# Performance work log

Measured on AMD Instinct MI355X. Metric: run time of the kernel, lower is better.

Reference implementation:

```python
import jax, jax.numpy as jnp
import numpy as np

N, E, DIN, H, C = 100000, 1600000, 128, 4, 32
NEG_SLOPE = 0.2

def setup_inputs() -> dict:
    key = jax.random.key(0)
    ks = jax.random.split(key, 6)
    x = jax.random.normal(ks[0], (N, DIN), jnp.float32)
    edge_index = jax.random.randint(ks[1], (2, E), 0, N)
    # positive scalar edge weights (log2 is applied to them)
    edge_attr = jax.random.uniform(ks[2], (E,), jnp.float32, 0.05, 1.0)
    scale = 1.0 / np.sqrt(DIN).astype(np.float32)
    W = jax.random.normal(ks[3], (DIN, H * C), jnp.float32) * scale
    att_src = jax.random.normal(ks[4], (H, C), jnp.float32) * scale
    att_dst = jax.random.normal(ks[5], (H, C), jnp.float32) * scale
    bias = jnp.zeros((H * C,), jnp.float32)
    return {"x": x, "edge_index": edge_index, "edge_attr": edge_attr,
            "W": W, "att_src": att_src, "att_dst": att_dst, "bias": bias}

def _gat_forward(x, edge_attr, W, att_src, att_dst, bias, src, dst):
    n = x.shape[0]
    h = (x @ W).reshape(n, H, C)                      # [N,H,C]
    a_src = jnp.einsum('nhc,hc->nh', h, att_src)      # [N,H]
    a_dst = jnp.einsum('nhc,hc->nh', h, att_dst)      # [N,H]
    # add self loops (pyg GATConv default), edge weight fill_value='mean' over incoming edges
    deg = jax.ops.segment_sum(jnp.ones_like(edge_attr), dst, n)
    loop_w = jnp.where(deg > 0,
                       jax.ops.segment_sum(edge_attr, dst, n) / jnp.maximum(deg, 1.0),
                       1.0)
    loops = jnp.arange(n)
    src_full = jnp.concatenate([src, loops])
    dst_full = jnp.concatenate([dst, loops])
    w_full = jnp.concatenate([edge_attr, loop_w])
    # per-edge attention logits
    alpha = jax.nn.leaky_relu(a_src[src_full] + a_dst[dst_full], NEG_SLOPE)
    alpha = alpha + jnp.log2(w_full)[:, None]         # [E+N, H]
    # segment (per-target-node) softmax
    amax = jax.ops.segment_max(alpha, dst_full, n)    # [N,H]; every node has a self loop
    ex = jnp.exp(alpha - amax[dst_full])
    denom = jax.ops.segment_sum(ex, dst_full, n)
    alpha = ex / denom[dst_full]                      # dropout is identity in eval mode
    # scatter-aggregate messages
    out = jax.ops.segment_sum(h[src_full] * alpha[:, :, None], dst_full, n)  # [N,H,C]
    return out.reshape(n, H * C) + bias

def reference(x, edge_index, edge_attr, W, att_src, att_dst, bias):
    src, dst = edge_index[0], edge_index[1]
    return _gat_forward(x, edge_attr, W, att_src, att_dst, bias, src, dst)
```

## Files before the change

### kernel.cpp

```cpp
#include <hip/hip_runtime.h>
#include <math.h>

#define DIN 128
#define NH 4
#define HC 128
static constexpr float NEG_SLOPE = 0.2f;

typedef __attribute__((ext_vector_type(8))) short bf16x8;
typedef __attribute__((ext_vector_type(4))) float f32x4;

__device__ __forceinline__ float leaky(float x) { return x > 0.f ? x : NEG_SLOPE * x; }

__device__ __forceinline__ unsigned short f2bf(float f) {
  unsigned u = __float_as_uint(f);
  unsigned r = (u + 0x7fffu + ((u >> 16) & 1u)) >> 16;
  return (unsigned short)r;
}
__device__ __forceinline__ float bf_lo(unsigned u) { return __uint_as_float(u << 16); }
__device__ __forceinline__ float bf_hi(unsigned u) { return __uint_as_float(u & 0xffff0000u); }

__global__ void k_init(const float* __restrict__ W, short* __restrict__ bswz,
                       unsigned* __restrict__ cnt, int n) {
  int g = blockIdx.x * blockDim.x + threadIdx.x;
  if (g < n) cnt[g] = 0u;
  if (g < 2048) {
    int ntile = g >> 8;
    int ks = (g >> 6) & 3;
    int lane = g & 63;
    int col = (ntile << 4) + (lane & 15);
    int kb = ks * 32 + ((lane >> 4) << 3);
    bf16x8 v;
#pragma unroll
    for (int j = 0; j < 8; ++j) v[j] = (short)f2bf(W[(kb + j) * HC + col]);
    ((bf16x8*)bswz)[g] = v;
  }
}

__global__ __launch_bounds__(256) void k_fused(
    const float* __restrict__ x, const short* __restrict__ bswz,
    const float* __restrict__ att_s, const float* __restrict__ att_d,
    unsigned short* __restrict__ hbf,
    float* __restrict__ a_src, float* __restrict__ a_dst, int n,
    const int* __restrict__ dst,
    unsigned* __restrict__ cnt, unsigned short* __restrict__ rank,
    int E, int CB) {
  int grp = blockIdx.x / 5;
  int r = blockIdx.x % 5;
  if (r >= 3) {
    int cid = grp * 2 + (r - 3);
    int stride = CB * 256;
    for (int e = cid * 256 + (int)threadIdx.x; e < E; e += stride) {
      unsigned old = atomicAdd(&cnt[dst[e]], 1u);
      rank[e] = (unsigned short)old;
    }
    return;
  }
  int pid = grp * 3 + r;
  int wtile = pid * 4 + (threadIdx.x >> 6);
  int ntiles = n >> 4;
  if (wtile >= ntiles) return;
  int lane = threadIdx.x & 63;
  int row0 = wtile << 4;

  int arow = row0 + (lane & 15);
  int kbase = (lane >> 4) << 3;
  const float* xr = x + (size_t)arow * DIN;
  bf16x8 a[4];
#pragma unroll
  for (int ks = 0; ks < 4; ++ks) {
    float4 lo = *(const float4*)(xr + ks * 32 + kbase);
    float4 hi = *(const float4*)(xr + ks * 32 + kbase + 4);
    bf16x8 v;
    v[0] = (short)f2bf(lo.x); v[1] = (short)f2bf(lo.y);
    v[2] = (short)f2bf(lo.z); v[3] = (short)f2bf(lo.w);
    v[4] = (short)f2bf(hi.x); v[5] = (short)f2bf(hi.y);
    v[6] = (short)f2bf(hi.z); v[7] = (short)f2bf(hi.w);
    a[ks] = v;
  }

  const bf16x8* B = (const bf16x8*)bswz;
  int crow_base = row0 + ((lane >> 4) << 2);
  int ccol_off = lane & 15;

  float ra[4] = {0.f, 0.f, 0.f, 0.f};
  float rd[4] = {0.f, 0.f, 0.f, 0.f};

#pragma unroll
  for (int ntile = 0; ntile < 8; ++ntile) {
    f32x4 acc = {0.f, 0.f, 0.f, 0.f};
#pragma unroll
    for (int ks = 0; ks < 4; ++ks)
      acc = __builtin_amdgcn_mfma_f32_16x16x32_bf16(a[ks], B[(ntile * 4 + ks) * 64 + lane], acc, 0, 0, 0);
    int col = (ntile << 4) + ccol_off;
    float as = att_s[col], ad = att_d[col];
#pragma unroll
    for (int i = 0; i < 4; ++i) {
      hbf[(size_t)(crow_base + i) * HC + col] = f2bf(acc[i]);
      ra[i] = fmaf(acc[i], as, ra[i]);
      rd[i] = fmaf(acc[i], ad, rd[i]);
    }
    if (ntile & 1) {
      int hh = ntile >> 1;
#pragma unroll
      for (int i = 0; i < 4; ++i) {
#pragma unroll
        for (int m = 1; m <= 8; m <<= 1) {
          ra[i] += __shfl_xor(ra[i], m, 64);
          rd[i] += __shfl_xor(rd[i], m, 64);
        }
        if ((lane & 15) == 0) {
          a_src[(crow_base + i) * NH + hh] = ra[i];
          a_dst[(crow_base + i) * NH + hh] = rd[i];
        }
        ra[i] = 0.f; rd[i] = 0.f;
      }
    }
  }
}

__global__ __launch_bounds__(256) void k_scan1(const unsigned* __restrict__ cnt,
                                               int* __restrict__ off,
                                               int* __restrict__ bsum, int n) {
  __shared__ int lds[256];
  int b = blockIdx.x, t = threadIdx.x;
  int base = b * 1024 + t * 4;
  int v0 = 0, v1 = 0, v2 = 0, v3 = 0;
  if (base + 0 < n) v0 = (int)cnt[base + 0];
  if (base + 1 < n) v1 = (int)cnt[base + 1];
  if (base + 2 < n) v2 = (int)cnt[base + 2];
  if (base + 3 < n) v3 = (int)cnt[base + 3];
  int s = v0 + v1 + v2 + v3;
  lds[t] = s;
  __syncthreads();
  for (int ofs = 1; ofs < 256; ofs <<= 1) {
    int x = (t >= ofs) ? lds[t - ofs] : 0;
    __syncthreads();
    lds[t] += x;
    __syncthreads();
  }
  int run = (t > 0) ? lds[t - 1] : 0;
  if (t == 255) bsum[b] = lds[255];
  if (base + 0 < n) { off[base + 0] = run; run += v0; }
  if (base + 1 < n) { off[base + 1] = run; run += v1; }
  if (base + 2 < n) { off[base + 2] = run; run += v2; }
  if (base + 3 < n) { off[base + 3] = run; run += v3; }
}

__global__ __launch_bounds__(256) void k_scan2(int* __restrict__ bsum, int nb) {
  __shared__ int lds[256];
  int t = threadIdx.x;
  lds[t] = (t < nb) ? bsum[t] : 0;
  __syncthreads();
  for (int ofs = 1; ofs < 256; ofs <<= 1) {
    int x = (t >= ofs) ? lds[t - ofs] : 0;
    __syncthreads();
    lds[t] += x;
    __syncthreads();
  }
  int excl = (t > 0) ? lds[t - 1] : 0;
  if (t < nb) bsum[t] = excl;
}

__global__ void k_scatter(const int* __restrict__ ei, const float* __restrict__ w,
                          const int* __restrict__ off, const int* __restrict__ bsum,
                          const unsigned short* __restrict__ rank,
                          int2* __restrict__ edges2, int E) {
  int e = blockIdx.x * blockDim.x + threadIdx.x;
  if (e >= E) return;
  int s = ei[e], d = ei[E + e];
  int p = off[d] + bsum[d >> 10] + (int)rank[e];
  edges2[p] = make_int2(s, __float_as_int(w[e]));
}

__global__ __launch_bounds__(256) void k_gather(
    const int2* __restrict__ edges2,
    const int* __restrict__ off, const int* __restrict__ bsum,
    const float* __restrict__ a_src, const float* __restrict__ a_dst,
    const unsigned short* __restrict__ hbf, const float* __restrict__ bias,
    float* __restrict__ out, int n, int E) {
  int node = blockIdx.x * 4 + (threadIdx.x >> 6);
  if (node >= n) return;
  int t = threadIdx.x & 63;
  int j2 = t * 2;
  int hh = t >> 4;
  int beg = off[node] + bsum[node >> 10];
  int end = (node == n - 1) ? E : off[node + 1] + bsum[(node + 1) >> 10];

  float adq = a_dst[node * NH + (t & 3)];
  float acc0 = 0.f, acc1 = 0.f, den = 0.f, wacc = 0.f;

  int c0 = beg;
  for (; c0 + 16 <= end; c0 += 16) {
    int2 ev = edges2[c0 + (t & 15)];
    int sq = __shfl(ev.x, t >> 2, 64);
    float wq = __int_as_float(__shfl(ev.y, t >> 2, 64));
    float asq = a_src[sq * NH + (t & 3)];
    float et = expf(leaky(asq + adq) + log2f(wq));
    wacc += ((t & 3) == 0) ? wq : 0.f;
#pragma unroll
    for (int j = 0; j < 16; ++j) {
      int s = __shfl(ev.x, j, 64);
      float e = __shfl(et, j * 4 + hh, 64);
      unsigned u = *(const unsigned*)(hbf + (size_t)s * HC + j2);
      den += e;
      acc0 = fmaf(e, bf_lo(u), acc0);
      acc1 = fmaf(e, bf_hi(u), acc1);
    }
  }
  int rem = end - c0;
  if (rem > 0) {
    int2 ev = make_int2(0, __float_as_int(1.0f));
    if ((t & 15) < rem) ev = edges2[c0 + (t & 15)];
    int q = t >> 2;
    int sq = __shfl(ev.x, q, 64);
    float wq = __int_as_float(__shfl(ev.y, q, 64));
    float asq = a_src[sq * NH + (t & 3)];
    float et = expf(leaky(asq + adq) + log2f(wq));
    wacc += ((t & 3) == 0 && q < rem) ? wq : 0.f;
    for (int j = 0; j < rem; ++j) {
      int s = __shfl(ev.x, j, 64);
      float e = __shfl(et, j * 4 + hh, 64);
      unsigned u = *(const unsigned*)(hbf + (size_t)s * HC + j2);
      den += e;
      acc0 = fmaf(e, bf_lo(u), acc0);
      acc1 = fmaf(e, bf_hi(u), acc1);
    }
  }

#pragma unroll
  for (int m = 1; m <= 32; m <<= 1) wacc += __shfl_xor(wacc, m, 64);

  int deg = end - beg;
  float lw = deg > 0 ? wacc / (float)deg : 1.f;
  float exs = expf(leaky(a_src[node * NH + hh] + a_dst[node * NH + hh]) + log2f(lw));
  den += exs;
  unsigned us = *(const unsigned*)(hbf + (size_t)node * HC + j2);
  acc0 = fmaf(exs, bf_lo(us), acc0);
  acc1 = fmaf(exs, bf_hi(us), acc1);
  float rden = 1.f / den;
  float2 o;
  o.x = acc0 * rden + bias[j2];
  o.y = acc1 * rden + bias[j2 + 1];
  *(float2*)(out + (size_t)node * HC + j2) = o;
}

extern "C" void kernel_launch(void* const* d_in, const int* in_sizes, int n_in,
                              void* d_out, int out_size, void* d_ws, size_t ws_size,
                              hipStream_t stream) {
  const float* x       = (const float*)d_in[0];
  const int*   ei      = (const int*)d_in[1];
  const float* eattr   = (const float*)d_in[2];
  const float* W       = (const float*)d_in[3];
  const float* att_src = (const float*)d_in[4];
  const float* att_dst = (const float*)d_in[5];
  const float* bias    = (const float*)d_in[6];
  float* out = (float*)d_out;

  const int n = in_sizes[0] / DIN;
  const int E = in_sizes[2];

  unsigned short* hbf = (unsigned short*)d_ws;
  int2*   edges2 = (int2*)(hbf + (size_t)n * HC);
  float*  a_src  = (float*)(edges2 + E);
  float*  a_dst  = a_src + (size_t)n * NH;
  short*  bswz   = (short*)(a_dst + (size_t)n * NH);
  unsigned* cnt  = (unsigned*)(bswz + 16384);
  int*    off    = (int*)(cnt + n);
  unsigned short* rank = (unsigned short*)(off + n + 1);
  int*    bsum   = (int*)(rank + E);

  const int* dst_idx = ei + E;
  int nb = (n + 1023) / 1024;
  int wavetiles = n >> 4;
  int PB = (wavetiles + 3) / 4;
  int PB3 = ((PB + 2) / 3) * 3;
  int CB = 2 * (PB3 / 3);
  int grid = PB3 + CB;

  k_init<<<(n + 255) / 256, 256, 0, stream>>>(W, bswz, cnt, n);
  k_fused<<<grid, 256, 0, stream>>>(x, bswz, att_src, att_dst, hbf, a_src, a_dst, n,
                                    dst_idx, cnt, rank, E, CB);
  k_scan1<<<nb, 256, 0, stream>>>(cnt, off, bsum, n);
  k_scan2<<<1, 256, 0, stream>>>(bsum, nb);
  k_scatter<<<(E + 255) / 256, 256, 0, stream>>>(ei, eattr, off, bsum, rank, edges2, E);
  k_gather<<<(n + 3) / 4, 256, 0, stream>>>(edges2, off, bsum, a_src, a_dst,
                                            hbf, bias, out, n, E);
}
```

Measured before the change: 213.1 us.

## Pad per-node CSR edge segments to multiples of 16 to drop gather remainder loop

The scan now rounds each node's in-degree up to a multiple of 16, so every edge segment is 16-aligned and zero-padded. Padding entries come from a memset and hold src 0 and weight 0, so their attention weight becomes exp(-inf)=0. The gather kernel then runs only fully unrolled 16-edge chunks, with no variable-length remainder loop, and reads the true degree from cnt. The cost is an extra memset of the enlarged edge buffer, more gather iterations over padded slots, and a larger, sparser scatter footprint.

```diff
diff --git a/kernel.cpp b/kernel.cpp
--- a/kernel.cpp
+++ b/kernel.cpp
@@ -125,10 +125,10 @@
   int b = blockIdx.x, t = threadIdx.x;
   int base = b * 1024 + t * 4;
   int v0 = 0, v1 = 0, v2 = 0, v3 = 0;
-  if (base + 0 < n) v0 = (int)cnt[base + 0];
-  if (base + 1 < n) v1 = (int)cnt[base + 1];
-  if (base + 2 < n) v2 = (int)cnt[base + 2];
-  if (base + 3 < n) v3 = (int)cnt[base + 3];
+  if (base + 0 < n) v0 = ((int)cnt[base + 0] + 15) & ~15;
+  if (base + 1 < n) v1 = ((int)cnt[base + 1] + 15) & ~15;
+  if (base + 2 < n) v2 = ((int)cnt[base + 2] + 15) & ~15;
+  if (base + 3 < n) v3 = ((int)cnt[base + 3] + 15) & ~15;
   int s = v0 + v1 + v2 + v3;
   lds[t] = s;
   __syncthreads();
@@ -175,28 +175,30 @@
 __global__ __launch_bounds__(256) void k_gather(
     const int2* __restrict__ edges2,
     const int* __restrict__ off, const int* __restrict__ bsum,
+    const unsigned* __restrict__ cnt,
     const float* __restrict__ a_src, const float* __restrict__ a_dst,
     const unsigned short* __restrict__ hbf, const float* __restrict__ bias,
-    float* __restrict__ out, int n, int E) {
+    float* __restrict__ out, int n) {
   int node = blockIdx.x * 4 + (threadIdx.x >> 6);
   if (node >= n) return;
   int t = threadIdx.x & 63;
   int j2 = t * 2;
   int hh = t >> 4;
+  int t15 = t & 15, q = t >> 2, h4 = t & 3;
   int beg = off[node] + bsum[node >> 10];
-  int end = (node == n - 1) ? E : off[node + 1] + bsum[(node + 1) >> 10];
-
-  float adq = a_dst[node * NH + (t & 3)];
+  int deg = (int)cnt[node];
+  int end = beg + ((deg + 15) & ~15);
+
+  float adq = a_dst[node * NH + h4];
   float acc0 = 0.f, acc1 = 0.f, den = 0.f, wacc = 0.f;
 
-  int c0 = beg;
-  for (; c0 + 16 <= end; c0 += 16) {
-    int2 ev = edges2[c0 + (t & 15)];
-    int sq = __shfl(ev.x, t >> 2, 64);
-    float wq = __int_as_float(__shfl(ev.y, t >> 2, 64));
-    float asq = a_src[sq * NH + (t & 3)];
+  for (int c = beg; c < end; c += 16) {
+    int2 ev = edges2[c + t15];
+    int sq = __shfl(ev.x, q, 64);
+    float wq = __int_as_float(__shfl(ev.y, q, 64));
+    float asq = a_src[sq * NH + h4];
     float et = expf(leaky(asq + adq) + log2f(wq));
-    wacc += ((t & 3) == 0) ? wq : 0.f;
+    wacc += (h4 == 0) ? wq : 0.f;
 #pragma unroll
     for (int j = 0; j < 16; ++j) {
       int s = __shfl(ev.x, j, 64);
@@ -207,30 +209,10 @@
       acc1 = fmaf(e, bf_hi(u), acc1);
     }
   }
-  int rem = end - c0;
-  if (rem > 0) {
-    int2 ev = make_int2(0, __float_as_int(1.0f));
-    if ((t & 15) < rem) ev = edges2[c0 + (t & 15)];
-    int q = t >> 2;
-    int sq = __shfl(ev.x, q, 64);
-    float wq = __int_as_float(__shfl(ev.y, q, 64));
-    float asq = a_src[sq * NH + (t & 3)];
-    float et = expf(leaky(asq + adq) + log2f(wq));
-    wacc += ((t & 3) == 0 && q < rem) ? wq : 0.f;
-    for (int j = 0; j < rem; ++j) {
-      int s = __shfl(ev.x, j, 64);
-      float e = __shfl(et, j * 4 + hh, 64);
-      unsigned u = *(const unsigned*)(hbf + (size_t)s * HC + j2);
-      den += e;
-      acc0 = fmaf(e, bf_lo(u), acc0);
-      acc1 = fmaf(e, bf_hi(u), acc1);
-    }
-  }
 
 #pragma unroll
   for (int m = 1; m <= 32; m <<= 1) wacc += __shfl_xor(wacc, m, 64);
 
-  int deg = end - beg;
   float lw = deg > 0 ? wacc / (float)deg : 1.f;
   float exs = expf(leaky(a_src[node * NH + hh] + a_dst[node * NH + hh]) + log2f(lw));
   den += exs;
@@ -258,15 +240,16 @@
 
   const int n = in_sizes[0] / DIN;
   const int E = in_sizes[2];
+  const size_t EPAD = (size_t)E + (size_t)n * 15;
 
   unsigned short* hbf = (unsigned short*)d_ws;
   int2*   edges2 = (int2*)(hbf + (size_t)n * HC);
-  float*  a_src  = (float*)(edges2 + E);
+  float*  a_src  = (float*)(edges2 + EPAD);
   float*  a_dst  = a_src + (size_t)n * NH;
   short*  bswz   = (short*)(a_dst + (size_t)n * NH);
   unsigned* cnt  = (unsigned*)(bswz + 16384);
   int*    off    = (int*)(cnt + n);
-  unsigned short* rank = (unsigned short*)(off + n + 1);
+  unsigned short* rank = (unsigned short*)(off + n);
   int*    bsum   = (int*)(rank + E);
 
   const int* dst_idx = ei + E;
@@ -277,12 +260,13 @@
   int CB = 2 * (PB3 / 3);
   int grid = PB3 + CB;
 
+  hipMemsetAsync(edges2, 0, EPAD * sizeof(int2), stream);
   k_init<<<(n + 255) / 256, 256, 0, stream>>>(W, bswz, cnt, n);
   k_fused<<<grid, 256, 0, stream>>>(x, bswz, att_src, att_dst, hbf, a_src, a_dst, n,
                                     dst_idx, cnt, rank, E, CB);
   k_scan1<<<nb, 256, 0, stream>>>(cnt, off, bsum, n);
   k_scan2<<<1, 256, 0, stream>>>(bsum, nb);
   k_scatter<<<(E + 255) / 256, 256, 0, stream>>>(ei, eattr, off, bsum, rank, edges2, E);
-  k_gather<<<(n + 3) / 4, 256, 0, stream>>>(edges2, off, bsum, a_src, a_dst,
-                                            hbf, bias, out, n, E);
-}
+  k_gather<<<(n + 3) / 4, 256, 0, stream>>>(edges2, off, bsum, cnt, a_src, a_dst,
+                                            hbf, bias, out, n);
+}
```

After: 196.9 us. 1.08x faster.
